# Optimization experiments

Measured on AMD Instinct MI355X. Metric: run time of the kernel, lower is better.

The kernel has to match this reference:

```python
import jax, jax.numpy as jnp
import numpy as np

L, D, H, F, V, B, S = 4, 256, 8, 2048, 1024, 4, 1024
HD = D // H
EPS = 1e-5
PARAM_NAMES = ['enc_qkv_w','enc_qkv_b','enc_out_w','enc_out_b','enc_ff1_w','enc_ff1_b','enc_ff2_w','enc_ff2_b','enc_ln1_g','enc_ln1_b','enc_ln2_g','enc_ln2_b','dec_sa_qkv_w','dec_sa_qkv_b','dec_sa_out_w','dec_sa_out_b','dec_ca_qkv_w','dec_ca_qkv_b','dec_ca_out_w','dec_ca_out_b','dec_ff1_w','dec_ff1_b','dec_ff2_w','dec_ff2_b','dec_ln1_g','dec_ln1_b','dec_ln2_g','dec_ln2_b','dec_ln3_g','dec_ln3_b']

def _ln(x, g, b):
    m = jnp.mean(x, -1, keepdims=True)
    v = jnp.mean((x - m) ** 2, -1, keepdims=True)
    return (x - m) * jax.lax.rsqrt(v + EPS) * g + b

def _mha(q_in, kv_in, qkv_w, qkv_b, out_w, out_b, key_mask=None):
    wq, wk, wv = jnp.split(qkv_w, 3, axis=0)
    bq, bk, bv = jnp.split(qkv_b, 3, axis=0)
    q = (q_in @ wq.T + bq).reshape(q_in.shape[0], -1, H, HD)
    k = (kv_in @ wk.T + bk).reshape(kv_in.shape[0], -1, H, HD)
    v = (kv_in @ wv.T + bv).reshape(kv_in.shape[0], -1, H, HD)
    scores = jnp.einsum('bqhd,bkhd->bhqk', q, k) / np.float32(np.sqrt(HD))
    if key_mask is not None:
        scores = jnp.where(key_mask[:, None, None, :], jnp.float32(-1e9), scores)
    attn = jax.nn.softmax(scores, axis=-1)
    o = jnp.einsum('bhqk,bkhd->bqhd', attn, v).reshape(q_in.shape[0], -1, D)
    return o @ out_w.T + out_b

def _forward(x, mask, codebook, pos, p):
    h = codebook[x] + pos[:, :x.shape[1], :]  # [B,S,D]
    # --- bidirectional encoder (post-LN, ReLU FFN, torch defaults) ---
    ctx = h
    for l in range(L):
        sa = _mha(ctx, ctx, p['enc_qkv_w'][l], p['enc_qkv_b'][l], p['enc_out_w'][l], p['enc_out_b'][l], mask)
        ctx = _ln(ctx + sa, p['enc_ln1_g'][l], p['enc_ln1_b'][l])
        ff = jax.nn.relu(ctx @ p['enc_ff1_w'][l].T + p['enc_ff1_b'][l]) @ p['enc_ff2_w'][l].T + p['enc_ff2_b'][l]
        ctx = _ln(ctx + ff, p['enc_ln2_g'][l], p['enc_ln2_b'][l])
    # --- depth decoder: original loops per position with tgt len 1.
    # Self-attn over a single token == out_proj(v_proj(x)); cross-attn over the
    # shared context is independent per position, so all S positions batch exactly. ---
    d = h
    for l in range(L):
        wv = p['dec_sa_qkv_w'][l][2 * D:]
        bv = p['dec_sa_qkv_b'][l][2 * D:]
        sa = (d @ wv.T + bv) @ p['dec_sa_out_w'][l].T + p['dec_sa_out_b'][l]
        d = _ln(d + sa, p['dec_ln1_g'][l], p['dec_ln1_b'][l])
        ca = _mha(d, ctx, p['dec_ca_qkv_w'][l], p['dec_ca_qkv_b'][l], p['dec_ca_out_w'][l], p['dec_ca_out_b'][l])
        d = _ln(d + ca, p['dec_ln2_g'][l], p['dec_ln2_b'][l])
        ff = jax.nn.relu(d @ p['dec_ff1_w'][l].T + p['dec_ff1_b'][l]) @ p['dec_ff2_w'][l].T + p['dec_ff2_b'][l]
        d = _ln(d + ff, p['dec_ln3_g'][l], p['dec_ln3_b'][l])
    return d

def setup_inputs() -> dict:
    key = jax.random.key(0)
    ctr = [0]
    def nk():
        k = jax.random.fold_in(key, ctr[0]); ctr[0] += 1; return k
    def prm(shape):
        return jax.random.normal(nk(), shape, jnp.float32) * 0.02
    inp = {
        'x': jax.random.randint(nk(), (B, S), 0, V),
        'mask': jnp.zeros((B, S), bool),
        'codebook': prm((V, D)),
        'pos': prm((1, V, D)),
        'enc_qkv_w': prm((L, 3 * D, D)), 'enc_qkv_b': jnp.zeros((L, 3 * D)),
        'enc_out_w': prm((L, D, D)), 'enc_out_b': jnp.zeros((L, D)),
        'enc_ff1_w': prm((L, F, D)), 'enc_ff1_b': jnp.zeros((L, F)),
        'enc_ff2_w': prm((L, D, F)), 'enc_ff2_b': jnp.zeros((L, D)),
        'enc_ln1_g': jnp.ones((L, D)), 'enc_ln1_b': jnp.zeros((L, D)),
        'enc_ln2_g': jnp.ones((L, D)), 'enc_ln2_b': jnp.zeros((L, D)),
        'dec_sa_qkv_w': prm((L, 3 * D, D)), 'dec_sa_qkv_b': jnp.zeros((L, 3 * D)),
        'dec_sa_out_w': prm((L, D, D)), 'dec_sa_out_b': jnp.zeros((L, D)),
        'dec_ca_qkv_w': prm((L, 3 * D, D)), 'dec_ca_qkv_b': jnp.zeros((L, 3 * D)),
        'dec_ca_out_w': prm((L, D, D)), 'dec_ca_out_b': jnp.zeros((L, D)),
        'dec_ff1_w': prm((L, F, D)), 'dec_ff1_b': jnp.zeros((L, F)),
        'dec_ff2_w': prm((L, D, F)), 'dec_ff2_b': jnp.zeros((L, D)),
        'dec_ln1_g': jnp.ones((L, D)), 'dec_ln1_b': jnp.zeros((L, D)),
        'dec_ln2_g': jnp.ones((L, D)), 'dec_ln2_b': jnp.zeros((L, D)),
        'dec_ln3_g': jnp.ones((L, D)), 'dec_ln3_b': jnp.zeros((L, D)),
    }
    return inp

def reference(x, mask, codebook, pos, enc_qkv_w, enc_qkv_b, enc_out_w, enc_out_b, enc_ff1_w, enc_ff1_b, enc_ff2_w, enc_ff2_b, enc_ln1_g, enc_ln1_b, enc_ln2_g, enc_ln2_b, dec_sa_qkv_w, dec_sa_qkv_b, dec_sa_out_w, dec_sa_out_b, dec_ca_qkv_w, dec_ca_qkv_b, dec_ca_out_w, dec_ca_out_b, dec_ff1_w, dec_ff1_b, dec_ff2_w, dec_ff2_b, dec_ln1_g, dec_ln1_b, dec_ln2_g, dec_ln2_b, dec_ln3_g, dec_ln3_b):
    vals = (enc_qkv_w, enc_qkv_b, enc_out_w, enc_out_b, enc_ff1_w, enc_ff1_b, enc_ff2_w, enc_ff2_b, enc_ln1_g, enc_ln1_b, enc_ln2_g, enc_ln2_b, dec_sa_qkv_w, dec_sa_qkv_b, dec_sa_out_w, dec_sa_out_b, dec_ca_qkv_w, dec_ca_qkv_b, dec_ca_out_w, dec_ca_out_b, dec_ff1_w, dec_ff1_b, dec_ff2_w, dec_ff2_b, dec_ln1_g, dec_ln1_b, dec_ln2_g, dec_ln2_b, dec_ln3_g, dec_ln3_b)
    p = dict(zip(PARAM_NAMES, vals))
    return _forward(x, mask, codebook, pos, p)
```

## Files before the change

kernel.cpp:

```cpp
#include <hip/hip_runtime.h>

typedef unsigned short u16;
typedef unsigned int   u32;
typedef short short8 __attribute__((ext_vector_type(8)));
typedef float f32x4  __attribute__((ext_vector_type(4)));

#define DEV static __device__ __forceinline__

static constexpr int S_ = 1024;
static constexpr int D_ = 256;
static constexpr int NR = 4096;

DEV u16 f2bf(float x) {
    u32 u = __float_as_uint(x);
    return (u16)((u + 0x7FFFu + ((u >> 16) & 1u)) >> 16);
}
DEV float bf2f(u16 s) { return __uint_as_float(((u32)s) << 16); }


__global__ __launch_bounds__(256) void k_fillf(float* __restrict__ o, int n, float v) {
    int i = blockIdx.x * 256 + threadIdx.x;
    if (i < n) o[i] = v;
}

__global__ __launch_bounds__(256) void k_conv_all(
        const float* __restrict__ s0, const float* __restrict__ s1, const float* __restrict__ s2,
        const float* __restrict__ s3, const float* __restrict__ s4, const float* __restrict__ s5,
        const float* __restrict__ s6, const float* __restrict__ s7, const float* __restrict__ s8,
        const float* __restrict__ s9, u16* __restrict__ dst) {
    constexpr int c0 = 786432/4,            c1 = c0 + 262144/4,  c2 = c1 + 2097152/4,
                  c3 = c2 + 2097152/4,      c4 = c3 + 786432/4,  c5 = c4 + 262144/4,
                  c6 = c5 + 786432/4,       c7 = c6 + 262144/4,  c8 = c7 + 2097152/4,
                  c9 = c8 + 2097152/4;
    for (int i = blockIdx.x * 256 + threadIdx.x; i < c9; i += gridDim.x * 256) {
        const float* src; int base;
        if      (i < c0) { src = s0; base = 0;  }
        else if (i < c1) { src = s1; base = c0; }
        else if (i < c2) { src = s2; base = c1; }
        else if (i < c3) { src = s3; base = c2; }
        else if (i < c4) { src = s4; base = c3; }
        else if (i < c5) { src = s5; base = c4; }
        else if (i < c6) { src = s6; base = c5; }
        else if (i < c7) { src = s7; base = c6; }
        else if (i < c8) { src = s8; base = c7; }
        else             { src = s9; base = c8; }
        float4 v = ((const float4*)src)[i - base];
        ushort4 o; o.x = f2bf(v.x); o.y = f2bf(v.y); o.z = f2bf(v.z); o.w = f2bf(v.w);
        ((ushort4*)dst)[i] = o;
    }
}

__global__ __launch_bounds__(256) void k_wsa(const float* __restrict__ qkvw, const float* __restrict__ qkvb,
                                             const float* __restrict__ outw, const float* __restrict__ outb,
                                             u16* __restrict__ wsa, float* __restrict__ bsa) {
    int l = blockIdx.x >> 8, n = blockIdx.x & 255, t = threadIdx.x;
    const float* wv = qkvw + (size_t)l * 196608 + 131072;
    const float* bv = qkvb + l * 768 + 512;
    const float* wo = outw + (size_t)l * 65536 + n * 256;
    float acc = 0.0f, pb = 0.0f;
    for (int j = 0; j < 256; j++) {
        float woj = wo[j];
        acc = fmaf(woj, wv[j * 256 + t], acc);
        pb  = fmaf(woj, bv[j], pb);
    }
    wsa[(size_t)l * 65536 + n * 256 + t] = f2bf(acc);
    if (t == 0) bsa[l * 256 + n] = pb + outb[l * 256 + n];
}

__global__ __launch_bounds__(256) void k_embed(const int* __restrict__ xx,
                                               const float* __restrict__ cb,
                                               const float* __restrict__ pos,
                                               const unsigned char* __restrict__ mask,
                                               float* __restrict__ hf, u16* __restrict__ hb,
                                               float* __restrict__ av, float* __restrict__ avz) {
    int wid = threadIdx.x >> 6, lane = threadIdx.x & 63;
    int row = blockIdx.x * 4 + wid;
    int sp = row & (S_ - 1);
    int tok = xx[row];
    float4 c = ((const float4*)(cb + (size_t)tok * D_))[lane];
    float4 p = ((const float4*)(pos + (size_t)sp * D_))[lane];
    float4 s; s.x = c.x + p.x; s.y = c.y + p.y; s.z = c.z + p.z; s.w = c.w + p.w;
    ((float4*)(hf + (size_t)row * D_))[lane] = s;
    ushort4 o; o.x = f2bf(s.x); o.y = f2bf(s.y); o.z = f2bf(s.z); o.w = f2bf(s.w);
    ((ushort4*)(hb + (size_t)row * D_))[lane] = o;
    if (lane == 0) { av[row] = mask[row] ? -2.0e9f : 0.0f; avz[row] = 0.0f; }
}

__global__ __launch_bounds__(256) void k_ln(const float* __restrict__ x, const float* __restrict__ y,
                                            const float* __restrict__ gg, const float* __restrict__ bb,
                                            float* __restrict__ of, u16* __restrict__ ob) {
    int wid = threadIdx.x >> 6, lane = threadIdx.x & 63;
    int row = blockIdx.x * 4 + wid;
    float4 xv = ((const float4*)(x + (size_t)row * D_))[lane];
    float4 yv = ((const float4*)(y + (size_t)row * D_))[lane];
    float4 s; s.x = xv.x + yv.x; s.y = xv.y + yv.y; s.z = xv.z + yv.z; s.w = xv.w + yv.w;
    float sum = s.x + s.y + s.z + s.w;
    float sq  = s.x * s.x + s.y * s.y + s.z * s.z + s.w * s.w;
    #pragma unroll
    for (int m = 1; m < 64; m <<= 1) { sum += __shfl_xor(sum, m, 64); sq += __shfl_xor(sq, m, 64); }
    float mean = sum * (1.0f / 256.0f);
    float var  = sq * (1.0f / 256.0f) - mean * mean;
    float rs = rsqrtf(var + 1e-5f);
    float4 gv = ((const float4*)gg)[lane];
    float4 bv = ((const float4*)bb)[lane];
    float4 o;
    o.x = (s.x - mean) * rs * gv.x + bv.x;
    o.y = (s.y - mean) * rs * gv.y + bv.y;
    o.z = (s.z - mean) * rs * gv.z + bv.z;
    o.w = (s.w - mean) * rs * gv.w + bv.w;
    ((float4*)(of + (size_t)row * D_))[lane] = o;
    ushort4 ub; ub.x = f2bf(o.x); ub.y = f2bf(o.y); ub.z = f2bf(o.z); ub.w = f2bf(o.w);
    ((ushort4*)(ob + (size_t)row * D_))[lane] = ub;
}

__global__ __launch_bounds__(256) void k_ln4(const float* __restrict__ x, const float* __restrict__ yp,
                                             const float* __restrict__ gg, const float* __restrict__ bb,
                                             float* __restrict__ of, u16* __restrict__ ob) {
    int wid = threadIdx.x >> 6, lane = threadIdx.x & 63;
    int row = blockIdx.x * 4 + wid;
    float4 xv = ((const float4*)(x + (size_t)row * D_))[lane];
    float4 s = xv;
    #pragma unroll
    for (int kz = 0; kz < 4; kz++) {
        float4 yv = ((const float4*)(yp + (size_t)kz * NR * D_ + (size_t)row * D_))[lane];
        s.x += yv.x; s.y += yv.y; s.z += yv.z; s.w += yv.w;
    }
    float sum = s.x + s.y + s.z + s.w;
    float sq  = s.x * s.x + s.y * s.y + s.z * s.z + s.w * s.w;
    #pragma unroll
    for (int m = 1; m < 64; m <<= 1) { sum += __shfl_xor(sum, m, 64); sq += __shfl_xor(sq, m, 64); }
    float mean = sum * (1.0f / 256.0f);
    float var  = sq * (1.0f / 256.0f) - mean * mean;
    float rs = rsqrtf(var + 1e-5f);
    float4 gv = ((const float4*)gg)[lane];
    float4 bv = ((const float4*)bb)[lane];
    float4 o;
    o.x = (s.x - mean) * rs * gv.x + bv.x;
    o.y = (s.y - mean) * rs * gv.y + bv.y;
    o.z = (s.z - mean) * rs * gv.z + bv.z;
    o.w = (s.w - mean) * rs * gv.w + bv.w;
    ((float4*)(of + (size_t)row * D_))[lane] = o;
    ushort4 ub; ub.x = f2bf(o.x); ub.y = f2bf(o.y); ub.z = f2bf(o.z); ub.w = f2bf(o.w);
    ((ushort4*)(ob + (size_t)row * D_))[lane] = ub;
}


template <int BM, int BN, bool RELU, bool OBF16>
__global__ __launch_bounds__(256) void k_gemm(const u16* __restrict__ A, const u16* __restrict__ Bw,
                                              const float* __restrict__ bias,
                                              float* __restrict__ Cf, u16* __restrict__ Cb,
                                              int Nn, int Kk) {
    constexpr int FM = BM / 32, FN = BN / 32;
    constexpr int LDA = 72;
    __shared__ __align__(16) u16 As[BM * LDA];
    __shared__ __align__(16) u16 Bs[BN * LDA];
    int tid = threadIdx.x, w = tid >> 6, lane = tid & 63;
    int lr = lane & 15, g = lane >> 4;
    int wm = w >> 1, wn = w & 1;
    int nbn = Nn / BN;
    int bid = blockIdx.x, nwg = gridDim.x;
    if ((nwg & 7) == 0) bid = (bid & 7) * (nwg >> 3) + (bid >> 3);
    int m0 = (bid / nbn) * BM, n0 = (bid % nbn) * BN;
    int trow = tid >> 3, tcol = (tid & 7) << 3;

    f32x4 acc[FM][FN] = {};

    for (int kb = 0; kb < Kk; kb += 64) {
        if (kb) __syncthreads();
        #pragma unroll
        for (int r = 0; r < BM / 32; r++) {
            int row = r * 32 + trow;
            uint4 v = *(const uint4*)(A + (size_t)(m0 + row) * Kk + kb + tcol);
            *(uint4*)(As + row * LDA + tcol) = v;
        }
        #pragma unroll
        for (int r = 0; r < BN / 32; r++) {
            int row = r * 32 + trow;
            uint4 v = *(const uint4*)(Bw + (size_t)(n0 + row) * Kk + kb + tcol);
            *(uint4*)(Bs + row * LDA + tcol) = v;
        }
        __syncthreads();
        #pragma unroll
        for (int kk = 0; kk < 2; kk++) {
            short8 af[FM], bfr[FN];
            #pragma unroll
            for (int mi = 0; mi < FM; mi++)
                af[mi] = *(const short8*)(As + (wm * (BM / 2) + mi * 16 + lr) * LDA + kk * 32 + g * 8);
            #pragma unroll
            for (int ni = 0; ni < FN; ni++)
                bfr[ni] = *(const short8*)(Bs + (wn * (BN / 2) + ni * 16 + lr) * LDA + kk * 32 + g * 8);
            #pragma unroll
            for (int mi = 0; mi < FM; mi++)
                #pragma unroll
                for (int ni = 0; ni < FN; ni++)
                    acc[mi][ni] = __builtin_amdgcn_mfma_f32_16x16x32_bf16(af[mi], bfr[ni], acc[mi][ni], 0, 0, 0);
        }
    }

    #pragma unroll
    for (int ni = 0; ni < FN; ni++) {
        int col = n0 + wn * (BN / 2) + ni * 16 + lr;
        float bi = bias[col];
        #pragma unroll
        for (int mi = 0; mi < FM; mi++) {
            #pragma unroll
            for (int jj = 0; jj < 4; jj++) {
                int row = m0 + wm * (BM / 2) + mi * 16 + g * 4 + jj;
                float v = acc[mi][ni][jj] + bi;
                if (RELU) v = fmaxf(v, 0.0f);
                if (OBF16) Cb[(size_t)row * Nn + col] = f2bf(v);
                else       Cf[(size_t)row * Nn + col] = v;
            }
        }
    }
}

__global__ __launch_bounds__(256) void k_gemm_sk4(const u16* __restrict__ A, const u16* __restrict__ Bw,
                                                  const float* __restrict__ bias, float* __restrict__ Cp) {
    constexpr int LDA = 72, Nn = 256, Kk = 2048;
    __shared__ __align__(16) u16 As[64 * LDA];
    __shared__ __align__(16) u16 Bs[64 * LDA];
    int tid = threadIdx.x, w = tid >> 6, lane = tid & 63;
    int lr = lane & 15, g = lane >> 4;
    int wm = w >> 1, wn = w & 1;
    int kz = blockIdx.x >> 8;
    int mn = blockIdx.x & 255;
    mn = (mn & 7) * 32 + (mn >> 3);
    int m0 = (mn >> 2) * 64, n0 = (mn & 3) * 64;
    int kbeg = kz * 512;
    int trow = tid >> 3, tcol = (tid & 7) << 3;

    f32x4 acc[2][2] = {};

    for (int kb = kbeg; kb < kbeg + 512; kb += 64) {
        if (kb != kbeg) __syncthreads();
        #pragma unroll
        for (int r = 0; r < 2; r++) {
            int row = r * 32 + trow;
            uint4 va = *(const uint4*)(A + (size_t)(m0 + row) * Kk + kb + tcol);
            *(uint4*)(As + row * LDA + tcol) = va;
            uint4 vb = *(const uint4*)(Bw + (size_t)(n0 + row) * Kk + kb + tcol);
            *(uint4*)(Bs + row * LDA + tcol) = vb;
        }
        __syncthreads();
        #pragma unroll
        for (int kk = 0; kk < 2; kk++) {
            short8 af[2], bfr[2];
            #pragma unroll
            for (int mi = 0; mi < 2; mi++)
                af[mi] = *(const short8*)(As + (wm * 32 + mi * 16 + lr) * LDA + kk * 32 + g * 8);
            #pragma unroll
            for (int ni = 0; ni < 2; ni++)
                bfr[ni] = *(const short8*)(Bs + (wn * 32 + ni * 16 + lr) * LDA + kk * 32 + g * 8);
            #pragma unroll
            for (int mi = 0; mi < 2; mi++)
                #pragma unroll
                for (int ni = 0; ni < 2; ni++)
                    acc[mi][ni] = __builtin_amdgcn_mfma_f32_16x16x32_bf16(af[mi], bfr[ni], acc[mi][ni], 0, 0, 0);
        }
    }

    float* Cz = Cp + (size_t)kz * NR * Nn;
    #pragma unroll
    for (int ni = 0; ni < 2; ni++) {
        int col = n0 + wn * 32 + ni * 16 + lr;
        float bi = (kz == 0) ? bias[col] : 0.0f;
        #pragma unroll
        for (int mi = 0; mi < 2; mi++)
            #pragma unroll
            for (int jj = 0; jj < 4; jj++) {
                int row = m0 + wm * 32 + mi * 16 + g * 4 + jj;
                Cz[(size_t)row * Nn + col] = acc[mi][ni][jj] + bi;
            }
    }
}


__global__ __launch_bounds__(256) void k_attn(const u16* __restrict__ qp, int qs,
                                              const u16* __restrict__ kvp, int ks, int koff, int voff,
                                              const float* __restrict__ addv, u16* __restrict__ out) {
    __shared__ __align__(16) u16 Kl[2][128 * 32];
    __shared__ __align__(16) u16 VTl[2][32 * 136];
    __shared__ __align__(16) u16 Pl[4 * 16 * 136];
    __shared__ float Al[2][128];

    int tid = threadIdx.x, w = tid >> 6, lane = tid & 63;
    int lr = lane & 15, g = lane >> 4;
    int blk = blockIdx.x;
    blk = (blk & 7) * 64 + (blk >> 3);
    int qb = blk & 15, h = (blk >> 4) & 7, b = blk >> 7;
    int q0 = qb * 64 + w * 16;
    const float QS = 0.17677669529663687f;

    short8 qf = *(const short8*)(qp + (size_t)(b * S_ + q0 + lr) * qs + h * 32 + g * 8);

    f32x4 o0 = {0.f, 0.f, 0.f, 0.f}, o1 = {0.f, 0.f, 0.f, 0.f};
    float m_run = -3.0e38f, l_run = 0.0f;
    float sreg[8][4];
    u16* Pw = Pl + w * 16 * 136;

    int key_t = tid >> 1, dh = (tid & 1) * 16;
    const u16* kbase = kvp + (size_t)(b * S_) * ks;

    uint4 ka0, ka1;
    union { uint4 v[2]; u16 s[16]; } vu;
    float alv = 0.0f;
    auto ldregs = [&](int kb) {
        const u16* srck = kbase + (size_t)(kb * 128 + key_t) * ks + koff + h * 32 + dh;
        ka0 = *(const uint4*)srck;
        ka1 = *(const uint4*)(srck + 8);
        const u16* srcv = kbase + (size_t)(kb * 128 + key_t) * ks + voff + h * 32 + dh;
        vu.v[0] = *(const uint4*)srcv;
        vu.v[1] = *(const uint4*)(srcv + 8);
        if (tid < 128) alv = addv[b * S_ + kb * 128 + tid];
    };
    auto stbuf = [&](int buf) {
        *(uint4*)(&Kl[buf][key_t * 32 + dh])     = ka0;
        *(uint4*)(&Kl[buf][key_t * 32 + dh + 8]) = ka1;
        #pragma unroll
        for (int i = 0; i < 16; i++) VTl[buf][(dh + i) * 136 + key_t] = vu.s[i];
        if (tid < 128) Al[buf][tid] = alv;
    };

    ldregs(0); stbuf(0);
    int cur = 0;
    for (int kb = 0; kb < 8; kb++) {
        __syncthreads();

        #pragma unroll
        for (int t = 0; t < 8; t++) {
            short8 kf = *(const short8*)(&Kl[cur][(t * 16 + lr) * 32 + g * 8]);
            f32x4 z = {0.f, 0.f, 0.f, 0.f};
            f32x4 st = __builtin_amdgcn_mfma_f32_16x16x32_bf16(kf, qf, z, 0, 0, 0);
            #pragma unroll
            for (int jj = 0; jj < 4; jj++) sreg[t][jj] = st[jj] * QS + Al[cur][t * 16 + g * 4 + jj];
        }

        if (kb < 7) ldregs(kb + 1);

        float mb = -3.0e38f;
        #pragma unroll
        for (int t = 0; t < 8; t++)
            #pragma unroll
            for (int jj = 0; jj < 4; jj++) mb = fmaxf(mb, sreg[t][jj]);
        mb = fmaxf(mb, __shfl_xor(mb, 16, 64));
        mb = fmaxf(mb, __shfl_xor(mb, 32, 64));
        float mnew = fmaxf(m_run, mb);
        float sc = __expf(m_run - mnew);
        float ls = 0.f;
        #pragma unroll
        for (int t = 0; t < 8; t++)
            #pragma unroll
            for (int jj = 0; jj < 4; jj++) {
                float p = __expf(sreg[t][jj] - mnew);
                sreg[t][jj] = p; ls += p;
            }
        ls += __shfl_xor(ls, 16, 64); ls += __shfl_xor(ls, 32, 64);
        l_run = l_run * sc + ls; m_run = mnew;
        #pragma unroll
        for (int jj = 0; jj < 4; jj++) {
            float scj = __shfl(sc, 20 * g + jj, 64);
            o0[jj] *= scj; o1[jj] *= scj;
        }

        #pragma unroll
        for (int t = 0; t < 8; t++) {
            u32 u0 = (u32)f2bf(sreg[t][0]) | ((u32)f2bf(sreg[t][1]) << 16);
            u32 u1 = (u32)f2bf(sreg[t][2]) | ((u32)f2bf(sreg[t][3]) << 16);
            *(uint2*)(Pw + lr * 136 + t * 16 + g * 4) = make_uint2(u0, u1);
        }

        #pragma unroll
        for (int c = 0; c < 4; c++) {
            short8 pa = *(const short8*)(Pw + lr * 136 + c * 32 + g * 8);
            short8 v0 = *(const short8*)(&VTl[cur][lr * 136 + c * 32 + g * 8]);
            short8 v1 = *(const short8*)(&VTl[cur][(16 + lr) * 136 + c * 32 + g * 8]);
            o0 = __builtin_amdgcn_mfma_f32_16x16x32_bf16(pa, v0, o0, 0, 0, 0);
            o1 = __builtin_amdgcn_mfma_f32_16x16x32_bf16(pa, v1, o1, 0, 0, 0);
        }

        __syncthreads();
        if (kb < 7) stbuf(cur ^ 1);
        cur ^= 1;
    }

    float li = 1.0f / l_run;
    #pragma unroll
    for (int jj = 0; jj < 4; jj++) {
        float lij = __shfl(li, 20 * g + jj, 64);
        int r = q0 + g * 4 + jj;
        u16* op = out + (size_t)(b * S_ + r) * 256 + h * 32;
        op[lr]      = f2bf(o0[jj] * lij);
        op[16 + lr] = f2bf(o1[jj] * lij);
    }
}


extern "C" void kernel_launch(void* const* d_in, const int* in_sizes, int n_in,
                              void* d_out, int out_size, void* d_ws, size_t ws_size,
                              hipStream_t stream) {
    const int* x                = (const int*)d_in[0];
    const unsigned char* mask   = (const unsigned char*)d_in[1];
    const float* codebook       = (const float*)d_in[2];
    const float* pos            = (const float*)d_in[3];
    const float* enc_qkv_w = (const float*)d_in[4];  const float* enc_qkv_b = (const float*)d_in[5];
    const float* enc_out_w = (const float*)d_in[6];  const float* enc_out_b = (const float*)d_in[7];
    const float* enc_ff1_w = (const float*)d_in[8];  const float* enc_ff1_b = (const float*)d_in[9];
    const float* enc_ff2_w = (const float*)d_in[10]; const float* enc_ff2_b = (const float*)d_in[11];
    const float* enc_ln1_g = (const float*)d_in[12]; const float* enc_ln1_b = (const float*)d_in[13];
    const float* enc_ln2_g = (const float*)d_in[14]; const float* enc_ln2_b = (const float*)d_in[15];
    const float* dec_sa_qkv_w = (const float*)d_in[16]; const float* dec_sa_qkv_b = (const float*)d_in[17];
    const float* dec_sa_out_w = (const float*)d_in[18]; const float* dec_sa_out_b = (const float*)d_in[19];
    const float* dec_ca_qkv_w = (const float*)d_in[20]; const float* dec_ca_qkv_b = (const float*)d_in[21];
    const float* dec_ca_out_w = (const float*)d_in[22]; const float* dec_ca_out_b = (const float*)d_in[23];
    const float* dec_ff1_w = (const float*)d_in[24]; const float* dec_ff1_b = (const float*)d_in[25];
    const float* dec_ff2_w = (const float*)d_in[26]; const float* dec_ff2_b = (const float*)d_in[27];
    const float* dec_ln1_g = (const float*)d_in[28]; const float* dec_ln1_b = (const float*)d_in[29];
    const float* dec_ln2_g = (const float*)d_in[30]; const float* dec_ln2_b = (const float*)d_in[31];
    const float* dec_ln3_g = (const float*)d_in[32]; const float* dec_ln3_b = (const float*)d_in[33];

    char* ws = (char*)d_ws; size_t off = 0;
    auto alloc = [&](size_t b) { char* p = ws + off; off += (b + 255) & ~(size_t)255; return p; };

    u16* w_eqkv  = (u16*)alloc((size_t)786432 * 2);
    u16* w_eout  = (u16*)alloc((size_t)262144 * 2);
    u16* w_eff1  = (u16*)alloc((size_t)2097152 * 2);
    u16* w_eff2  = (u16*)alloc((size_t)2097152 * 2);
    u16* w_dsaq  = (u16*)alloc((size_t)786432 * 2);
    u16* w_dsao  = (u16*)alloc((size_t)262144 * 2);
    u16* w_dcaq  = (u16*)alloc((size_t)786432 * 2);
    u16* w_dcao  = (u16*)alloc((size_t)262144 * 2);
    u16* w_dff1  = (u16*)alloc((size_t)2097152 * 2);
    u16* w_dff2  = (u16*)alloc((size_t)2097152 * 2);
    u16*   wsa   = (u16*)  alloc((size_t)4 * 65536 * 2);
    float* bsa   = (float*)alloc((size_t)4 * 256 * 4);
    float* h_f   = (float*)alloc((size_t)NR * D_ * 4);
    u16*   h_b   = (u16*)  alloc((size_t)NR * D_ * 2);
    float* ctx_f = (float*)alloc((size_t)NR * D_ * 4);
    u16*   ctx_b = (u16*)  alloc((size_t)NR * D_ * 2);
    float* dd_f  = (float*)alloc((size_t)NR * D_ * 4);
    u16*   dd_b  = (u16*)  alloc((size_t)NR * D_ * 2);
    float* gem_f = (float*)alloc((size_t)NR * 256 * 4);
    float* gem_p = (float*)alloc((size_t)4 * NR * 256 * 4);
    u16*   attno = (u16*)  alloc((size_t)NR * 256 * 2);
    float* addv  = (float*)alloc((size_t)NR * 4);
    float* addvz = (float*)alloc((size_t)NR * 4);
    u16* scr = (u16*)alloc((size_t)NR * 2048 * 2);
    u16* qkv_b = scr;
    u16* ffh_b = scr;
    u16* qca_b = scr;
    u16* kvca_b = scr + (size_t)NR * 256;
    (void)in_sizes; (void)n_in;

    if (off > ws_size) {
        k_fillf<<<(out_size + 255) / 256, 256, 0, stream>>>((float*)d_out, out_size, 1000.0f);
        return;
    }

    k_conv_all<<<2048, 256, 0, stream>>>(enc_qkv_w, enc_out_w, enc_ff1_w, enc_ff2_w,
                                         dec_sa_qkv_w, dec_sa_out_w, dec_ca_qkv_w, dec_ca_out_w,
                                         dec_ff1_w, dec_ff2_w, w_eqkv);
    k_wsa<<<1024, 256, 0, stream>>>(dec_sa_qkv_w, dec_sa_qkv_b, dec_sa_out_w, dec_sa_out_b, wsa, bsa);
    k_embed<<<1024, 256, 0, stream>>>(x, codebook, pos, mask, h_f, h_b, addv, addvz);

    for (int l = 0; l < 4; l++) {
        const u16* inb = l ? ctx_b : h_b;
        const float* inf = l ? ctx_f : h_f;
        k_gemm<128,128,false,true><<<192, 256, 0, stream>>>(inb, w_eqkv + (size_t)l*196608,
            enc_qkv_b + l*768, nullptr, qkv_b, 768, 256);
        k_attn<<<512, 256, 0, stream>>>(qkv_b, 768, qkv_b, 768, 256, 512, addv, attno);
        k_gemm<64,64,false,false><<<256, 256, 0, stream>>>(attno, w_eout + (size_t)l*65536,
            enc_out_b + l*256, gem_f, nullptr, 256, 256);
        k_ln<<<1024, 256, 0, stream>>>(inf, gem_f, enc_ln1_g + l*256, enc_ln1_b + l*256, ctx_f, ctx_b);
        k_gemm<128,128,true,true><<<512, 256, 0, stream>>>(ctx_b, w_eff1 + (size_t)l*524288,
            enc_ff1_b + l*2048, nullptr, ffh_b, 2048, 256);
        k_gemm_sk4<<<1024, 256, 0, stream>>>(ffh_b, w_eff2 + (size_t)l*524288,
            enc_ff2_b + l*256, gem_p);
        k_ln4<<<1024, 256, 0, stream>>>(ctx_f, gem_p, enc_ln2_g + l*256, enc_ln2_b + l*256, ctx_f, ctx_b);
    }

    for (int l = 0; l < 4; l++) {
        const u16* inb = l ? dd_b : h_b;
        const float* inf = l ? dd_f : h_f;
        k_gemm<64,64,false,false><<<256, 256, 0, stream>>>(inb, wsa + (size_t)l*65536,
            bsa + l*256, gem_f, nullptr, 256, 256);
        k_ln<<<1024, 256, 0, stream>>>(inf, gem_f, dec_ln1_g + l*256, dec_ln1_b + l*256, dd_f, dd_b);
        k_gemm<64,64,false,true><<<256, 256, 0, stream>>>(dd_b, w_dcaq + (size_t)l*196608,
            dec_ca_qkv_b + l*768, nullptr, qca_b, 256, 256);
        k_gemm<64,64,false,true><<<512, 256, 0, stream>>>(ctx_b, w_dcaq + (size_t)l*196608 + 65536,
            dec_ca_qkv_b + l*768 + 256, nullptr, kvca_b, 512, 256);
        k_attn<<<512, 256, 0, stream>>>(qca_b, 256, kvca_b, 512, 0, 256, addvz, attno);
        k_gemm<64,64,false,false><<<256, 256, 0, stream>>>(attno, w_dcao + (size_t)l*65536,
            dec_ca_out_b + l*256, gem_f, nullptr, 256, 256);
        k_ln<<<1024, 256, 0, stream>>>(dd_f, gem_f, dec_ln2_g + l*256, dec_ln2_b + l*256, dd_f, dd_b);
        k_gemm<128,128,true,true><<<512, 256, 0, stream>>>(dd_b, w_dff1 + (size_t)l*524288,
            dec_ff1_b + l*2048, nullptr, ffh_b, 2048, 256);
        k_gemm_sk4<<<1024, 256, 0, stream>>>(ffh_b, w_dff2 + (size_t)l*524288,
            dec_ff2_b + l*256, gem_p);
        k_ln4<<<1024, 256, 0, stream>>>(dd_f, gem_p, dec_ln3_g + l*256, dec_ln3_b + l*256,
                                        (l == 3) ? (float*)d_out : dd_f, dd_b);
    }
}
```

Baseline: 620.9 us.

## Store split-K partials in bf16, fuse cross-attn QKV GEMMs, use exp2 softmax

```diff
diff --git a/kernel.cpp b/kernel.cpp
--- a/kernel.cpp
+++ b/kernel.cpp
@@ -113,7 +113,7 @@
     ((ushort4*)(ob + (size_t)row * D_))[lane] = ub;
 }
 
-__global__ __launch_bounds__(256) void k_ln4(const float* __restrict__ x, const float* __restrict__ yp,
+__global__ __launch_bounds__(256) void k_ln4(const float* __restrict__ x, const u16* __restrict__ yp,
                                              const float* __restrict__ gg, const float* __restrict__ bb,
                                              float* __restrict__ of, u16* __restrict__ ob) {
     int wid = threadIdx.x >> 6, lane = threadIdx.x & 63;
@@ -122,8 +122,8 @@
     float4 s = xv;
     #pragma unroll
     for (int kz = 0; kz < 4; kz++) {
-        float4 yv = ((const float4*)(yp + (size_t)kz * NR * D_ + (size_t)row * D_))[lane];
-        s.x += yv.x; s.y += yv.y; s.z += yv.z; s.w += yv.w;
+        ushort4 yv = ((const ushort4*)(yp + (size_t)kz * NR * D_ + (size_t)row * D_))[lane];
+        s.x += bf2f(yv.x); s.y += bf2f(yv.y); s.z += bf2f(yv.z); s.w += bf2f(yv.w);
     }
     float sum = s.x + s.y + s.z + s.w;
     float sq  = s.x * s.x + s.y * s.y + s.z * s.z + s.w * s.w;
@@ -215,8 +215,70 @@
     }
 }
 
+__global__ __launch_bounds__(256) void k_gemm2(const u16* __restrict__ A0, const u16* __restrict__ W0,
+                                               const float* __restrict__ b0, u16* __restrict__ C0,
+                                               const u16* __restrict__ A1, const u16* __restrict__ W1,
+                                               const float* __restrict__ b1, u16* __restrict__ C1) {
+    constexpr int LDA = 72, Kk = 256;
+    __shared__ __align__(16) u16 As[64 * LDA];
+    __shared__ __align__(16) u16 Bs[64 * LDA];
+    int tid = threadIdx.x, w = tid >> 6, lane = tid & 63;
+    int lr = lane & 15, g = lane >> 4;
+    int wm = w >> 1, wn = w & 1;
+    int bid = blockIdx.x;
+    bid = (bid & 7) * 96 + (bid >> 3);
+    const u16 *A, *Bw; const float* bias; u16* Cb; int Nn, nbn, seg;
+    if (bid < 256) { A = A0; Bw = W0; bias = b0; Cb = C0; Nn = 256; nbn = 4; seg = bid; }
+    else           { A = A1; Bw = W1; bias = b1; Cb = C1; Nn = 512; nbn = 8; seg = bid - 256; }
+    int m0 = (seg / nbn) * 64, n0 = (seg % nbn) * 64;
+    int trow = tid >> 3, tcol = (tid & 7) << 3;
+
+    f32x4 acc[2][2] = {};
+
+    for (int kb = 0; kb < Kk; kb += 64) {
+        if (kb) __syncthreads();
+        #pragma unroll
+        for (int r = 0; r < 2; r++) {
+            int row = r * 32 + trow;
+            uint4 va = *(const uint4*)(A + (size_t)(m0 + row) * Kk + kb + tcol);
+            *(uint4*)(As + row * LDA + tcol) = va;
+            uint4 vb = *(const uint4*)(Bw + (size_t)(n0 + row) * Kk + kb + tcol);
+            *(uint4*)(Bs + row * LDA + tcol) = vb;
+        }
+        __syncthreads();
+        #pragma unroll
+        for (int kk = 0; kk < 2; kk++) {
+            short8 af[2], bfr[2];
+            #pragma unroll
+            for (int mi = 0; mi < 2; mi++)
+                af[mi] = *(const short8*)(As + (wm * 32 + mi * 16 + lr) * LDA + kk * 32 + g * 8);
+            #pragma unroll
+            for (int ni = 0; ni < 2; ni++)
+                bfr[ni] = *(const short8*)(Bs + (wn * 32 + ni * 16 + lr) * LDA + kk * 32 + g * 8);
+            #pragma unroll
+            for (int mi = 0; mi < 2; mi++)
+                #pragma unroll
+                for (int ni = 0; ni < 2; ni++)
+                    acc[mi][ni] = __builtin_amdgcn_mfma_f32_16x16x32_bf16(af[mi], bfr[ni], acc[mi][ni], 0, 0, 0);
+        }
+    }
+
+    #pragma unroll
+    for (int ni = 0; ni < 2; ni++) {
+        int col = n0 + wn * 32 + ni * 16 + lr;
+        float bi = bias[col];
+        #pragma unroll
+        for (int mi = 0; mi < 2; mi++)
+            #pragma unroll
+            for (int jj = 0; jj < 4; jj++) {
+                int row = m0 + wm * 32 + mi * 16 + g * 4 + jj;
+                Cb[(size_t)row * Nn + col] = f2bf(acc[mi][ni][jj] + bi);
+            }
+    }
+}
+
 __global__ __launch_bounds__(256) void k_gemm_sk4(const u16* __restrict__ A, const u16* __restrict__ Bw,
-                                                  const float* __restrict__ bias, float* __restrict__ Cp) {
+                                                  const float* __restrict__ bias, u16* __restrict__ Cp) {
     constexpr int LDA = 72, Nn = 256, Kk = 2048;
     __shared__ __align__(16) u16 As[64 * LDA];
     __shared__ __align__(16) u16 Bs[64 * LDA];
@@ -260,7 +322,7 @@
         }
     }
 
-    float* Cz = Cp + (size_t)kz * NR * Nn;
+    u16* Cz = Cp + (size_t)kz * NR * Nn;
     #pragma unroll
     for (int ni = 0; ni < 2; ni++) {
         int col = n0 + wn * 32 + ni * 16 + lr;
@@ -270,7 +332,7 @@
             #pragma unroll
             for (int jj = 0; jj < 4; jj++) {
                 int row = m0 + wm * 32 + mi * 16 + g * 4 + jj;
-                Cz[(size_t)row * Nn + col] = acc[mi][ni][jj] + bi;
+                Cz[(size_t)row * Nn + col] = f2bf(acc[mi][ni][jj] + bi);
             }
     }
 }
@@ -290,7 +352,7 @@
     blk = (blk & 7) * 64 + (blk >> 3);
     int qb = blk & 15, h = (blk >> 4) & 7, b = blk >> 7;
     int q0 = qb * 64 + w * 16;
-    const float QS = 0.17677669529663687f;
+    const float QS2 = 0.17677669529663687f * 1.4426950408889634f;
 
     short8 qf = *(const short8*)(qp + (size_t)(b * S_ + q0 + lr) * qs + h * 32 + g * 8);
 
@@ -333,7 +395,7 @@
             f32x4 z = {0.f, 0.f, 0.f, 0.f};
             f32x4 st = __builtin_amdgcn_mfma_f32_16x16x32_bf16(kf, qf, z, 0, 0, 0);
             #pragma unroll
-            for (int jj = 0; jj < 4; jj++) sreg[t][jj] = st[jj] * QS + Al[cur][t * 16 + g * 4 + jj];
+            for (int jj = 0; jj < 4; jj++) sreg[t][jj] = st[jj] * QS2 + Al[cur][t * 16 + g * 4 + jj];
         }
 
         if (kb < 7) ldregs(kb + 1);
@@ -346,13 +408,13 @@
         mb = fmaxf(mb, __shfl_xor(mb, 16, 64));
         mb = fmaxf(mb, __shfl_xor(mb, 32, 64));
         float mnew = fmaxf(m_run, mb);
-        float sc = __expf(m_run - mnew);
+        float sc = __builtin_amdgcn_exp2f(m_run - mnew);
         float ls = 0.f;
         #pragma unroll
         for (int t = 0; t < 8; t++)
             #pragma unroll
             for (int jj = 0; jj < 4; jj++) {
-                float p = __expf(sreg[t][jj] - mnew);
+                float p = __builtin_amdgcn_exp2f(sreg[t][jj] - mnew);
                 sreg[t][jj] = p; ls += p;
             }
         ls += __shfl_xor(ls, 16, 64); ls += __shfl_xor(ls, 32, 64);
@@ -441,7 +503,7 @@
     float* dd_f  = (float*)alloc((size_t)NR * D_ * 4);
     u16*   dd_b  = (u16*)  alloc((size_t)NR * D_ * 2);
     float* gem_f = (float*)alloc((size_t)NR * 256 * 4);
-    float* gem_p = (float*)alloc((size_t)4 * NR * 256 * 4);
+    u16*   gem_p = (u16*)  alloc((size_t)4 * NR * 256 * 2);
     u16*   attno = (u16*)  alloc((size_t)NR * 256 * 2);
     float* addv  = (float*)alloc((size_t)NR * 4);
     float* addvz = (float*)alloc((size_t)NR * 4);
@@ -466,7 +528,7 @@
     for (int l = 0; l < 4; l++) {
         const u16* inb = l ? ctx_b : h_b;
         const float* inf = l ? ctx_f : h_f;
-        k_gemm<128,128,false,true><<<192, 256, 0, stream>>>(inb, w_eqkv + (size_t)l*196608,
+        k_gemm<64,64,false,true><<<768, 256, 0, stream>>>(inb, w_eqkv + (size_t)l*196608,
             enc_qkv_b + l*768, nullptr, qkv_b, 768, 256);
         k_attn<<<512, 256, 0, stream>>>(qkv_b, 768, qkv_b, 768, 256, 512, addv, attno);
         k_gemm<64,64,false,false><<<256, 256, 0, stream>>>(attno, w_eout + (size_t)l*65536,
@@ -485,10 +547,9 @@
         k_gemm<64,64,false,false><<<256, 256, 0, stream>>>(inb, wsa + (size_t)l*65536,
             bsa + l*256, gem_f, nullptr, 256, 256);
         k_ln<<<1024, 256, 0, stream>>>(inf, gem_f, dec_ln1_g + l*256, dec_ln1_b + l*256, dd_f, dd_b);
-        k_gemm<64,64,false,true><<<256, 256, 0, stream>>>(dd_b, w_dcaq + (size_t)l*196608,
-            dec_ca_qkv_b + l*768, nullptr, qca_b, 256, 256);
-        k_gemm<64,64,false,true><<<512, 256, 0, stream>>>(ctx_b, w_dcaq + (size_t)l*196608 + 65536,
-            dec_ca_qkv_b + l*768 + 256, nullptr, kvca_b, 512, 256);
+        k_gemm2<<<768, 256, 0, stream>>>(dd_b, w_dcaq + (size_t)l*196608, dec_ca_qkv_b + l*768, qca_b,
+                                         ctx_b, w_dcaq + (size_t)l*196608 + 65536,
+                                         dec_ca_qkv_b + l*768 + 256, kvca_b);
         k_attn<<<512, 256, 0, stream>>>(qca_b, 256, kvca_b, 512, 0, 256, addvz, attno);
         k_gemm<64,64,false,false><<<256, 256, 0, stream>>>(attno, w_dcao + (size_t)l*65536,
             dec_ca_out_b + l*256, gem_f, nullptr, 256, 256);
```

New measurement: 601.3 us. 1.03x faster.
